# Optimization experiments

Measured on AMD Instinct MI355X. Metric: run time of the kernel, lower is better.

The kernel has to match this reference:

```python
import jax, jax.numpy as jnp
import numpy as np

GROUP_SIZE = 128  # in_features // scales.shape[1]


def setup_inputs() -> dict:
    key = jax.random.key(0)
    kA, kq, ks, kz, kb = jax.random.split(key, 5)
    M, K, N = 2048, 4096, 4096
    G = K // GROUP_SIZE  # 32 groups
    A = jax.random.normal(kA, (M, K), dtype=jnp.float32)
    # unpacked uint4 quantized weights, values in [0, 16)
    qweight = jax.random.randint(kq, (N, K), 0, 16, dtype=jnp.int32)
    # per-group scales (typical GPTQ magnitude) and zero-points (float, 'original' zeros_mode)
    scales = jax.random.uniform(ks, (N, G), dtype=jnp.float32) * 0.02
    zeros = jax.random.uniform(kz, (N, G), dtype=jnp.float32) * 15.0
    bias = jax.random.normal(kb, (N,), dtype=jnp.float32)
    return {"A": A, "qweight": qweight, "scales": scales, "zeros": zeros, "bias": bias}


def reference(A, qweight, scales, zeros, bias):
    # Dequant: W[n,k] = (q[n,k] - zeros[n, k//gs]) * scales[n, k//gs]
    N, K = qweight.shape
    gs = K // scales.shape[1]
    s = jnp.repeat(scales, gs, axis=1)  # [N, K]
    z = jnp.repeat(zeros, gs, axis=1)   # [N, K]
    W = (qweight.astype(A.dtype) - z) * s
    # out[m,n] = sum_k A[m,k] * W[n,k] + bias[n]
    return jnp.einsum("mk,nk->mn", A, W) + bias
```

## Files before the change

### kernel.cpp

```cpp
#include <hip/hip_runtime.h>
#include <cstdint>
#include <cstddef>

#define MM 2048
#define KK 4096
#define NN 4096
#define GG 32
#define BM 128
#define BN 128
#define BK 64

typedef _Float16 half8_t __attribute__((ext_vector_type(8)));
typedef _Float16 half4_t __attribute__((ext_vector_type(4)));
typedef float f32x4 __attribute__((ext_vector_type(4)));

__device__ __forceinline__ void load_lds16(const void* gptr, void* lptr) {
  __builtin_amdgcn_global_load_lds(
      (const __attribute__((address_space(1))) unsigned int*)gptr,
      (__attribute__((address_space(3))) unsigned int*)lptr, 16, 0, 0);
}

#define ACNT (MM * KK / 4)
__global__ void prep_kernel(const float* __restrict__ A, const int* __restrict__ q,
                            const float* __restrict__ scales, const float* __restrict__ zeros,
                            _Float16* __restrict__ Ah, _Float16* __restrict__ Wh) {
  const int i = blockIdx.x * blockDim.x + threadIdx.x;
  if (i < ACNT) {
    const float4 v = ((const float4*)A)[i];
    half4_t h;
    h[0] = (_Float16)v.x; h[1] = (_Float16)v.y; h[2] = (_Float16)v.z; h[3] = (_Float16)v.w;
    *(half4_t*)(Ah + 4 * (size_t)i) = h;
  } else {
    const int j = i - ACNT;
    const int e = j << 2;
    const int n = e >> 12;
    const int k = e & (KK - 1);
    const int g = k >> 7;
    const float sc = scales[(n << 5) + g];
    const float zp = zeros[(n << 5) + g];
    const float nzs = -zp * sc;
    const int4 qv = ((const int4*)q)[j];
    half4_t h;
    h[0] = (_Float16)fmaf((float)qv.x, sc, nzs);
    h[1] = (_Float16)fmaf((float)qv.y, sc, nzs);
    h[2] = (_Float16)fmaf((float)qv.z, sc, nzs);
    h[3] = (_Float16)fmaf((float)qv.w, sc, nzs);
    *(half4_t*)(Wh + (size_t)e) = h;
  }
}

template <bool FUSED>
__global__ __launch_bounds__(256, 2)
void gemm_kernel(const _Float16* __restrict__ Ah, const _Float16* __restrict__ Wh,
                 const float* __restrict__ Af, const int* __restrict__ qw,
                 const float* __restrict__ scales, const float* __restrict__ zeros,
                 const float* __restrict__ bias, float* __restrict__ out)
{
  __shared__ __align__(16) _Float16 sA[BM * BK];
  __shared__ __align__(16) _Float16 sB[BN * BK];

  const int tid = threadIdx.x;
  const int lane = tid & 63;
  const int wave = tid >> 6;
  const int wr = wave >> 1, wc = wave & 1;

  const int bid = blockIdx.x;
  const int xcd = bid & 7;
  const int slot = bid >> 3;
  const int mt = slot >> 2;
  const int nt = xcd * 4 + (slot & 3);
  const int m0 = mt * BM;
  const int n0 = nt * BN;

  const int lr = lane & 15, quad = lane >> 4;

  f32x4 acc[4][4];
#pragma unroll
  for (int i = 0; i < 4; ++i)
#pragma unroll
    for (int j = 0; j < 4; ++j) acc[i][j] = (f32x4){0.f, 0.f, 0.f, 0.f};

  const int srow = lane >> 3;
  const int scc = lane & 7;
  const int gchunk = scc ^ srow;

  const int frow = tid >> 4;
  const int fc4 = tid & 15;

  for (int kt = 0; kt < KK / BK; ++kt) {
    const int k0 = kt * BK;
    if constexpr (!FUSED) {
#pragma unroll
      for (int i = 0; i < 4; ++i) {
        const int c = i * 4 + wave;
        const int row = c * 8 + srow;
        load_lds16(Ah + (size_t)(m0 + row) * KK + k0 + gchunk * 8, (void*)&sA[c * 512]);
        load_lds16(Wh + (size_t)(n0 + row) * KK + k0 + gchunk * 8, (void*)&sB[c * 512]);
      }
    } else {
      const int g = k0 >> 7;
#pragma unroll
      for (int p = 0; p < 8; ++p) {
        const int row = p * 16 + frow;
        const int pc = (fc4 >> 1) ^ (row & 7);
        const int dst = row * 64 + pc * 8 + (fc4 & 1) * 4;
        const float4 avf = *(const float4*)&Af[(size_t)(m0 + row) * KK + k0 + fc4 * 4];
        half4_t ah;
        ah[0] = (_Float16)avf.x; ah[1] = (_Float16)avf.y;
        ah[2] = (_Float16)avf.z; ah[3] = (_Float16)avf.w;
        *(half4_t*)&sA[dst] = ah;
        const int n = n0 + row;
        const float sc = scales[(n << 5) + g];
        const float zp = zeros[(n << 5) + g];
        const float nzs = -zp * sc;
        const int4 qv = *(const int4*)&qw[(size_t)n * KK + k0 + fc4 * 4];
        half4_t bh;
        bh[0] = (_Float16)fmaf((float)qv.x, sc, nzs);
        bh[1] = (_Float16)fmaf((float)qv.y, sc, nzs);
        bh[2] = (_Float16)fmaf((float)qv.z, sc, nzs);
        bh[3] = (_Float16)fmaf((float)qv.w, sc, nzs);
        *(half4_t*)&sB[dst] = bh;
      }
    }
    __syncthreads();
#pragma unroll
    for (int ks = 0; ks < 2; ++ks) {
      half8_t a[4], b[4];
#pragma unroll
      for (int t = 0; t < 4; ++t) {
        const int rA = wr * 64 + t * 16 + lr;
        const int j = ks * 4 + quad;
        a[t] = *(const half8_t*)&sA[rA * 64 + ((j ^ (lr & 7)) * 8)];
        const int rB = wc * 64 + t * 16 + lr;
        b[t] = *(const half8_t*)&sB[rB * 64 + ((j ^ (lr & 7)) * 8)];
      }
#pragma unroll
      for (int mi = 0; mi < 4; ++mi)
#pragma unroll
        for (int ni = 0; ni < 4; ++ni)
          acc[mi][ni] = __builtin_amdgcn_mfma_f32_16x16x32_f16(a[mi], b[ni], acc[mi][ni], 0, 0, 0);
    }
    __syncthreads();
  }

#pragma unroll
  for (int ni = 0; ni < 4; ++ni) {
    const int n = n0 + wc * 64 + ni * 16 + lr;
    const float bv = bias[n];
#pragma unroll
    for (int mi = 0; mi < 4; ++mi) {
      const int mbase = m0 + wr * 64 + mi * 16 + quad * 4;
#pragma unroll
      for (int r = 0; r < 4; ++r)
        out[(size_t)(mbase + r) * NN + n] = acc[mi][ni][r] + bv;
    }
  }
}

extern "C" void kernel_launch(void* const* d_in, const int* in_sizes, int n_in,
                              void* d_out, int out_size, void* d_ws, size_t ws_size,
                              hipStream_t stream) {
  (void)in_sizes; (void)n_in; (void)out_size;
  const float* A      = (const float*)d_in[0];
  const int*   qw     = (const int*)d_in[1];
  const float* scales = (const float*)d_in[2];
  const float* zeros  = (const float*)d_in[3];
  const float* bias   = (const float*)d_in[4];
  float* out = (float*)d_out;

  const size_t needA = (size_t)MM * KK * sizeof(_Float16);
  const size_t needW = (size_t)NN * KK * sizeof(_Float16);

  dim3 grid(NN / BN * MM / BM);
  dim3 block(256);

  if (ws_size >= needA + needW) {
    _Float16* Ah = (_Float16*)d_ws;
    _Float16* Wh = (_Float16*)((char*)d_ws + needA);
    prep_kernel<<<((MM + NN) * KK / 4) / 256, 256, 0, stream>>>(A, qw, scales, zeros, Ah, Wh);
    gemm_kernel<false><<<grid, block, 0, stream>>>(Ah, Wh, A, qw, scales, zeros, bias, out);
  } else {
    gemm_kernel<true><<<grid, block, 0, stream>>>(nullptr, nullptr, A, qw, scales, zeros, bias, out);
  }
}
```

Before: 204.5 us.

## Warp-specialize GEMM with producer waves and double-buffered LDS via flags

Replaces the single-buffer GEMM with a 512-thread block in which four producer waves issue global-to-LDS loads into a double buffer, while four consumer waves run the MFMAs. The two groups hand off through LDS atomic counters with sleep-polling instead of block-wide barriers. The goal is to overlap tile loads with compute. In exchange it spends waves on loading, doubles LDS use, and relies on hand-coded waitcnt values and spin loops, which may be fragile or add latency. The fused fallback path is kept as a separate kernel with a simpler block mapping.

```diff
diff --git a/kernel.cpp b/kernel.cpp
--- a/kernel.cpp
+++ b/kernel.cpp
@@ -9,6 +9,7 @@
 #define BM 128
 #define BN 128
 #define BK 64
+#define NKT (KK / BK)
 
 typedef _Float16 half8_t __attribute__((ext_vector_type(8)));
 typedef _Float16 half4_t __attribute__((ext_vector_type(4)));
@@ -49,100 +50,172 @@
   }
 }
 
-template <bool FUSED>
+__global__ __launch_bounds__(512, 4)
+void gemm_pipe(const _Float16* __restrict__ Ah, const _Float16* __restrict__ Wh,
+               const float* __restrict__ bias, float* __restrict__ out)
+{
+  __shared__ __align__(16) _Float16 sA[2][BM * BK];
+  __shared__ __align__(16) _Float16 sB[2][BN * BK];
+  __shared__ int flg[4];
+
+  const int tid = threadIdx.x;
+  const int lane = tid & 63;
+  const int wave = tid >> 6;
+
+  if (tid == 0) { flg[0] = 0; flg[1] = 0; flg[2] = 0; flg[3] = 0; }
+  __syncthreads();
+
+  const int bid = blockIdx.x;
+  const int xcd = bid & 7;
+  const int slot = bid >> 3;
+  const int m0 = (slot >> 2) * BM;
+  const int n0 = (xcd * 4 + (slot & 3)) * BN;
+
+  if (wave >= 4) {
+    const int pw = wave - 4;
+    const int srow = lane >> 3;
+    const int scc = lane & 7;
+    const int gchunk = scc ^ srow;
+    for (int t = 0; t < NKT; ++t) {
+      const int b = t & 1;
+      const int k0 = t * BK;
+      const int need = 4 * (t >> 1);
+      while (__hip_atomic_load(&flg[2 + b], __ATOMIC_ACQUIRE,
+                               __HIP_MEMORY_SCOPE_WORKGROUP) < need)
+        __builtin_amdgcn_s_sleep(1);
+#pragma unroll
+      for (int i = 0; i < 4; ++i) {
+        const int c = i * 4 + pw;
+        const int row = c * 8 + srow;
+        load_lds16(Ah + (size_t)(m0 + row) * KK + k0 + gchunk * 8, (void*)&sA[b][c * 512]);
+        load_lds16(Wh + (size_t)(n0 + row) * KK + k0 + gchunk * 8, (void*)&sB[b][c * 512]);
+      }
+      __builtin_amdgcn_s_waitcnt(0x0f70);
+      if (lane == 0)
+        __hip_atomic_fetch_add(&flg[b], 1, __ATOMIC_RELEASE,
+                               __HIP_MEMORY_SCOPE_WORKGROUP);
+    }
+    return;
+  }
+
+  const int wr = wave >> 1, wc = wave & 1;
+  const int lr = lane & 15, quad = lane >> 4;
+
+  f32x4 acc[4][4];
+#pragma unroll
+  for (int i = 0; i < 4; ++i)
+#pragma unroll
+    for (int j = 0; j < 4; ++j) acc[i][j] = (f32x4){0.f, 0.f, 0.f, 0.f};
+
+  for (int t = 0; t < NKT; ++t) {
+    const int b = t & 1;
+    const int need = 4 * ((t >> 1) + 1);
+    while (__hip_atomic_load(&flg[b], __ATOMIC_ACQUIRE,
+                             __HIP_MEMORY_SCOPE_WORKGROUP) < need)
+      __builtin_amdgcn_s_sleep(1);
+#pragma unroll
+    for (int ks = 0; ks < 2; ++ks) {
+      half8_t a[4], bfr[4];
+#pragma unroll
+      for (int tt = 0; tt < 4; ++tt) {
+        const int rA = wr * 64 + tt * 16 + lr;
+        const int j = ks * 4 + quad;
+        a[tt] = *(const half8_t*)&sA[b][rA * 64 + ((j ^ (lr & 7)) * 8)];
+        const int rB = wc * 64 + tt * 16 + lr;
+        bfr[tt] = *(const half8_t*)&sB[b][rB * 64 + ((j ^ (lr & 7)) * 8)];
+      }
+#pragma unroll
+      for (int mi = 0; mi < 4; ++mi)
+#pragma unroll
+        for (int ni = 0; ni < 4; ++ni)
+          acc[mi][ni] = __builtin_amdgcn_mfma_f32_16x16x32_f16(a[mi], bfr[ni], acc[mi][ni], 0, 0, 0);
+    }
+    __builtin_amdgcn_s_waitcnt(0xc07f);
+    if (lane == 0)
+      __hip_atomic_fetch_add(&flg[2 + b], 1, __ATOMIC_RELEASE,
+                             __HIP_MEMORY_SCOPE_WORKGROUP);
+  }
+
+#pragma unroll
+  for (int ni = 0; ni < 4; ++ni) {
+    const int n = n0 + wc * 64 + ni * 16 + lr;
+    const float bv = bias[n];
+#pragma unroll
+    for (int mi = 0; mi < 4; ++mi) {
+      const int mbase = m0 + wr * 64 + mi * 16 + quad * 4;
+#pragma unroll
+      for (int r = 0; r < 4; ++r)
+        out[(size_t)(mbase + r) * NN + n] = acc[mi][ni][r] + bv;
+    }
+  }
+}
+
 __global__ __launch_bounds__(256, 2)
-void gemm_kernel(const _Float16* __restrict__ Ah, const _Float16* __restrict__ Wh,
-                 const float* __restrict__ Af, const int* __restrict__ qw,
-                 const float* __restrict__ scales, const float* __restrict__ zeros,
-                 const float* __restrict__ bias, float* __restrict__ out)
+void gemm_fused(const float* __restrict__ Af, const int* __restrict__ qw,
+                const float* __restrict__ scales, const float* __restrict__ zeros,
+                const float* __restrict__ bias, float* __restrict__ out)
 {
   __shared__ __align__(16) _Float16 sA[BM * BK];
   __shared__ __align__(16) _Float16 sB[BN * BK];
-
   const int tid = threadIdx.x;
   const int lane = tid & 63;
   const int wave = tid >> 6;
   const int wr = wave >> 1, wc = wave & 1;
-
-  const int bid = blockIdx.x;
-  const int xcd = bid & 7;
-  const int slot = bid >> 3;
-  const int mt = slot >> 2;
-  const int nt = xcd * 4 + (slot & 3);
-  const int m0 = mt * BM;
-  const int n0 = nt * BN;
-
+  const int m0 = (blockIdx.x >> 5) * BM;
+  const int n0 = (blockIdx.x & 31) * BN;
   const int lr = lane & 15, quad = lane >> 4;
-
   f32x4 acc[4][4];
 #pragma unroll
   for (int i = 0; i < 4; ++i)
 #pragma unroll
     for (int j = 0; j < 4; ++j) acc[i][j] = (f32x4){0.f, 0.f, 0.f, 0.f};
-
-  const int srow = lane >> 3;
-  const int scc = lane & 7;
-  const int gchunk = scc ^ srow;
-
   const int frow = tid >> 4;
   const int fc4 = tid & 15;
-
-  for (int kt = 0; kt < KK / BK; ++kt) {
+  for (int kt = 0; kt < NKT; ++kt) {
     const int k0 = kt * BK;
-    if constexpr (!FUSED) {
-#pragma unroll
-      for (int i = 0; i < 4; ++i) {
-        const int c = i * 4 + wave;
-        const int row = c * 8 + srow;
-        load_lds16(Ah + (size_t)(m0 + row) * KK + k0 + gchunk * 8, (void*)&sA[c * 512]);
-        load_lds16(Wh + (size_t)(n0 + row) * KK + k0 + gchunk * 8, (void*)&sB[c * 512]);
+    const int g = k0 >> 7;
+#pragma unroll
+    for (int p = 0; p < 8; ++p) {
+      const int row = p * 16 + frow;
+      const int pc = (fc4 >> 1) ^ (row & 7);
+      const int dst = row * 64 + pc * 8 + (fc4 & 1) * 4;
+      const float4 avf = *(const float4*)&Af[(size_t)(m0 + row) * KK + k0 + fc4 * 4];
+      half4_t ah;
+      ah[0] = (_Float16)avf.x; ah[1] = (_Float16)avf.y;
+      ah[2] = (_Float16)avf.z; ah[3] = (_Float16)avf.w;
+      *(half4_t*)&sA[dst] = ah;
+      const int n = n0 + row;
+      const float sc = scales[(n << 5) + g];
+      const float zp = zeros[(n << 5) + g];
+      const float nzs = -zp * sc;
+      const int4 qv = *(const int4*)&qw[(size_t)n * KK + k0 + fc4 * 4];
+      half4_t bh;
+      bh[0] = (_Float16)fmaf((float)qv.x, sc, nzs);
+      bh[1] = (_Float16)fmaf((float)qv.y, sc, nzs);
+      bh[2] = (_Float16)fmaf((float)qv.z, sc, nzs);
+      bh[3] = (_Float16)fmaf((float)qv.w, sc, nzs);
+      *(half4_t*)&sB[dst] = bh;
+    }
+    __syncthreads();
+#pragma unroll
+    for (int ks = 0; ks < 2; ++ks) {
+      half8_t a[4], bfr[4];
+#pragma unroll
+      for (int tt = 0; tt < 4; ++tt) {
+        const int rA = wr * 64 + tt * 16 + lr;
+        const int j = ks * 4 + quad;
+        a[tt] = *(const half8_t*)&sA[rA * 64 + ((j ^ (lr & 7)) * 8)];
+        const int rB = wc * 64 + tt * 16 + lr;
+        bfr[tt] = *(const half8_t*)&sB[rB * 64 + ((j ^ (lr & 7)) * 8)];
       }
-    } else {
-      const int g = k0 >> 7;
-#pragma unroll
-      for (int p = 0; p < 8; ++p) {
-        const int row = p * 16 + frow;
-        const int pc = (fc4 >> 1) ^ (row & 7);
-        const int dst = row * 64 + pc * 8 + (fc4 & 1) * 4;
-        const float4 avf = *(const float4*)&Af[(size_t)(m0 + row) * KK + k0 + fc4 * 4];
-        half4_t ah;
-        ah[0] = (_Float16)avf.x; ah[1] = (_Float16)avf.y;
-        ah[2] = (_Float16)avf.z; ah[3] = (_Float16)avf.w;
-        *(half4_t*)&sA[dst] = ah;
-        const int n = n0 + row;
-        const float sc = scales[(n << 5) + g];
-        const float zp = zeros[(n << 5) + g];
-        const float nzs = -zp * sc;
-        const int4 qv = *(const int4*)&qw[(size_t)n * KK + k0 + fc4 * 4];
-        half4_t bh;
-        bh[0] = (_Float16)fmaf((float)qv.x, sc, nzs);
-        bh[1] = (_Float16)fmaf((float)qv.y, sc, nzs);
-        bh[2] = (_Float16)fmaf((float)qv.z, sc, nzs);
-        bh[3] = (_Float16)fmaf((float)qv.w, sc, nzs);
-        *(half4_t*)&sB[dst] = bh;
-      }
+#pragma unroll
+      for (int mi = 0; mi < 4; ++mi)
+#pragma unroll
+        for (int ni = 0; ni < 4; ++ni)
+          acc[mi][ni] = __builtin_amdgcn_mfma_f32_16x16x32_f16(a[mi], bfr[ni], acc[mi][ni], 0, 0, 0);
     }
     __syncthreads();
-#pragma unroll
-    for (int ks = 0; ks < 2; ++ks) {
-      half8_t a[4], b[4];
-#pragma unroll
-      for (int t = 0; t < 4; ++t) {
-        const int rA = wr * 64 + t * 16 + lr;
-        const int j = ks * 4 + quad;
-        a[t] = *(const half8_t*)&sA[rA * 64 + ((j ^ (lr & 7)) * 8)];
-        const int rB = wc * 64 + t * 16 + lr;
-        b[t] = *(const half8_t*)&sB[rB * 64 + ((j ^ (lr & 7)) * 8)];
-      }
-#pragma unroll
-      for (int mi = 0; mi < 4; ++mi)
-#pragma unroll
-        for (int ni = 0; ni < 4; ++ni)
-          acc[mi][ni] = __builtin_amdgcn_mfma_f32_16x16x32_f16(a[mi], b[ni], acc[mi][ni], 0, 0, 0);
-    }
-    __syncthreads();
-  }
-
+  }
 #pragma unroll
   for (int ni = 0; ni < 4; ++ni) {
     const int n = n0 + wc * 64 + ni * 16 + lr;
@@ -171,15 +244,12 @@
   const size_t needA = (size_t)MM * KK * sizeof(_Float16);
   const size_t needW = (size_t)NN * KK * sizeof(_Float16);
 
-  dim3 grid(NN / BN * MM / BM);
-  dim3 block(256);
-
   if (ws_size >= needA + needW) {
     _Float16* Ah = (_Float16*)d_ws;
     _Float16* Wh = (_Float16*)((char*)d_ws + needA);
     prep_kernel<<<((MM + NN) * KK / 4) / 256, 256, 0, stream>>>(A, qw, scales, zeros, Ah, Wh);
-    gemm_kernel<false><<<grid, block, 0, stream>>>(Ah, Wh, A, qw, scales, zeros, bias, out);
+    gemm_pipe<<<dim3(NN / BN * MM / BM), dim3(512), 0, stream>>>(Ah, Wh, bias, out);
   } else {
-    gemm_kernel<true><<<grid, block, 0, stream>>>(nullptr, nullptr, A, qw, scales, zeros, bias, out);
-  }
-}
+    gemm_fused<<<dim3(NN / BN * MM / BM), dim3(256), 0, stream>>>(A, qw, scales, zeros, bias, out);
+  }
+}
```

New measurement: 205.9 us. Within noise of the previous version (+0.7%).
